# Optimization experiments

Hardware: AMD Instinct MI355X
Metric: run time of the kernel (lower is better)

## Reference

```python
import jax, jax.numpy as jnp
import numpy as np

M, K, N, GROUP = 64, 4096, 11008, 128
NGROUPS = K // GROUP  # 32


def setup_inputs() -> dict:
    key = jax.random.key(0)
    k1, k2, k3, k4, k5 = jax.random.split(key, 5)
    x = jax.random.normal(k1, (M, K), dtype=jnp.float32)
    # packed int4 weights: 8 nibbles per int32, full 32-bit entropy
    qweight = jax.random.bits(k2, (K // 8, N), dtype=jnp.uint32).astype(jnp.int32)
    qzeros = jax.random.bits(k3, (NGROUPS, N // 8), dtype=jnp.uint32).astype(jnp.int32)
    scales = jax.random.uniform(k4, (NGROUPS, N), dtype=jnp.float32, minval=0.001, maxval=0.02)
    bias = jax.random.normal(k5, (N,), dtype=jnp.float32) * 0.01
    return {"x": x, "qweight": qweight, "qzeros": qzeros, "scales": scales, "bias": bias}


def dequantize(qweight, qzeros, scales):
    shifts = jnp.arange(8, dtype=jnp.int32) * 4  # nibble bit offsets 0..28
    # unpack weights: [K//8, N] -> [K//8, 8, N] -> [NGROUPS, GROUP, N]
    w = (jnp.right_shift(qweight[:, None, :], shifts[None, :, None]) & 15)
    w = w.reshape(-1, GROUP, qweight.shape[1])
    # unpack zeros: [NGROUPS, N//8] -> [NGROUPS, N//8, 8] -> [NGROUPS, 1, N]; GPTQ stores zero-1
    z = (jnp.right_shift(qzeros[:, :, None], shifts[None, None, :]) & 15) + 1
    z = z.reshape(z.shape[0], 1, -1)
    # scale * (q - zero), per group: [NGROUPS, GROUP, N] -> [K, N]
    W = scales[:, None, :] * (w - z).astype(scales.dtype)
    return W.reshape(-1, W.shape[2])


def reference(x, qweight, qzeros, scales, bias):
    W = dequantize(qweight, qzeros, scales)  # [K, N] fp32
    return jnp.matmul(x, W.astype(x.dtype)) + bias
```

## Files before the change

### kernel.cpp

```cpp
#include <hip/hip_runtime.h>
#include <hip/hip_bf16.h>

namespace {

constexpr int MM = 64;
constexpr int KK = 4096;
constexpr int NN = 11008;
constexpr int NZROW = NN / 8;
constexpr int BCOL = 128;
constexpr int KSPLIT = 8;
constexpr int KSEG = KK / KSPLIT;
constexpr int BK = 32;
constexpr int NCH = KSEG / BK;
constexpr int NG = KSEG / 128;
constexpr int NT = NN / BCOL;
constexpr int NCHT = KK / BK;
constexpr size_t XBT_OFF = (size_t)KSPLIT * MM * NN * 4;
constexpr size_t WS_NEED = XBT_OFF + (size_t)MM * KK * 2;

typedef float f32x4 __attribute__((ext_vector_type(4)));
typedef short s16x8 __attribute__((ext_vector_type(8)));
typedef int   i32x4 __attribute__((ext_vector_type(4)));

__device__ __forceinline__ int pack_bf16(float a, float b) {
  union { __hip_bfloat162 h; int i; } u;
  u.h.x = __float2bfloat16(a);
  u.h.y = __float2bfloat16(b);
  return u.i;
}

__global__ __launch_bounds__(256) void xcvt_kernel(
    const float* __restrict__ x, unsigned short* __restrict__ xbt)
{
  const int tg = blockIdx.x * 256 + threadIdx.x;
  const int l  = tg & 63;
  const int r  = (tg >> 6) & 3;
  const int ci = tg >> 8;
  const int m  = r * 16 + (l & 15);
  const int k  = ci * BK + (l >> 4) * 8;
  const float* xp = x + (size_t)m * KK + k;
  const f32x4 a0 = *(const f32x4*)xp;
  const f32x4 a1 = *(const f32x4*)(xp + 4);
  i32x4 p;
  p.x = pack_bf16(a0.x, a0.y);
  p.y = pack_bf16(a0.z, a0.w);
  p.z = pack_bf16(a1.x, a1.y);
  p.w = pack_bf16(a1.z, a1.w);
  *(i32x4*)(xbt + (size_t)tg * 8) = p;
}

__global__ __launch_bounds__(256) void prep_kernel(
    const float* __restrict__ bias, float* __restrict__ out)
{
  const int i = blockIdx.x * 256 + threadIdx.x;
  out[i] = bias[i % NN];
}

__global__ __launch_bounds__(256) void reduce_kernel(
    const float* __restrict__ ws, const float* __restrict__ bias,
    float* __restrict__ out)
{
  const int i4 = (blockIdx.x * 256 + threadIdx.x) * 4;
  f32x4 acc = *(const f32x4*)(bias + (i4 % NN));
  #pragma unroll
  for (int s = 0; s < KSPLIT; ++s)
    acc += *(const f32x4*)(ws + (size_t)s * (MM * NN) + i4);
  *(f32x4*)(out + i4) = acc;
}

template<bool WSP>
__global__ __launch_bounds__(256, 4) void gptq_gemm_kernel(
    const float* __restrict__ x, const int* __restrict__ qw,
    const int* __restrict__ qz, const float* __restrict__ scales,
    const unsigned short* __restrict__ xbt, float* __restrict__ out)
{
  const int tid  = threadIdx.x;
  const int wave = tid >> 6;
  const int lane = tid & 63;
  const int c    = lane & 15;
  const int quad = lane >> 4;

  const int ks     = blockIdx.x & 7;
  const int nt     = blockIdx.x >> 3;
  const int n0     = nt * BCOL;
  const int kbase0 = ks * KSEG;
  const int grp0   = kbase0 >> 7;

  const int ncol = n0 + wave * 32 + c;

  const int* qwb = qw + ((size_t)(kbase0 >> 3) + quad) * NN + ncol;
  const unsigned short* xbb = xbt + (size_t)(ks * NCH) * 2048 + lane * 8;
  const float* xab = x + (size_t)c * KK + kbase0 + quad * 8;

  f32x4 acc[8];
  #pragma unroll
  for (int t = 0; t < 8; ++t) acc[t] = {0.f, 0.f, 0.f, 0.f};

  s16x8 pA[2][4];
  int   pB0[4], pB1[4];
  float pS0[2], pS1[2];
  int   pZ0[2], pZ1[2];
  float s0, s1, C0, C1;

  auto ldA = [&](int i) {
    const unsigned short* xp = xbb + (size_t)i * 2048;
    #pragma unroll
    for (int r = 0; r < 4; ++r)
      pA[i & 1][r] = *(const s16x8*)(xp + r * 512);
  };
  auto pfB = [&](int i) {
    const int* qp = qwb + (size_t)i * 4 * NN;
    pB0[i & 3] = qp[0];
    pB1[i & 3] = qp[16];
  };
  auto pfS = [&](int g) {
    const int sl = g & 1;
    const float* sp = scales + (size_t)(grp0 + g) * NN + ncol;
    pS0[sl] = sp[0];
    pS1[sl] = sp[16];
    const int* zp = qz + (size_t)(grp0 + g) * NZROW + (ncol >> 3);
    pZ0[sl] = zp[0];
    pZ1[sl] = zp[2];
  };
  auto setSC = [&](int g) {
    const int sl = g & 1;
    const int sh = (ncol & 7) * 4;
    s0 = pS0[sl];
    s1 = pS1[sl];
    C0 = __int_as_float(0x4B000000 + ((pZ0[sl] >> sh) & 15) + 1);
    C1 = __int_as_float(0x4B000000 + ((pZ1[sl] >> sh) & 15) + 1);
  };
  auto dq8 = [&](int v, float s, float C) -> i32x4 {
    i32x4 p;
    p.x = pack_bf16(s * (__int_as_float(((v      ) & 15) | 0x4B000000) - C),
                    s * (__int_as_float(((v >>  4) & 15) | 0x4B000000) - C));
    p.y = pack_bf16(s * (__int_as_float(((v >>  8) & 15) | 0x4B000000) - C),
                    s * (__int_as_float(((v >> 12) & 15) | 0x4B000000) - C));
    p.z = pack_bf16(s * (__int_as_float(((v >> 16) & 15) | 0x4B000000) - C),
                    s * (__int_as_float(((v >> 20) & 15) | 0x4B000000) - C));
    p.w = pack_bf16(s * (__int_as_float(((v >> 24) & 15) | 0x4B000000) - C),
                    s * (__int_as_float(((v >> 28) & 15) | 0x4B000000) - C));
    return p;
  };
  auto ldA_f32 = [&](int i, int r) -> s16x8 {
    const float* xa = xab + (size_t)r * 16 * KK + i * BK;
    const f32x4 a0 = *(const f32x4*)xa;
    const f32x4 a1 = *(const f32x4*)(xa + 4);
    union { i32x4 i4; s16x8 s8; } ua;
    ua.i4.x = pack_bf16(a0.x, a0.y);
    ua.i4.y = pack_bf16(a0.z, a0.w);
    ua.i4.z = pack_bf16(a1.x, a1.y);
    ua.i4.w = pack_bf16(a1.z, a1.w);
    return ua.s8;
  };

  pfS(0);
  pfB(0); pfB(1); pfB(2);
  if (WSP) ldA(0);
  setSC(0);
  pfS(1);

  #pragma unroll
  for (int i = 0; i < NCH; ++i) {
    if (WSP && i + 1 < NCH) ldA(i + 1);
    if (i + 3 < NCH) pfB(i + 3);

    union { i32x4 i4; s16x8 s8; } u0, u1;
    u0.i4 = dq8(pB0[i & 3], s0, C0);
    u1.i4 = dq8(pB1[i & 3], s1, C1);

    #pragma unroll
    for (int r = 0; r < 4; ++r) {
      const s16x8 af = WSP ? pA[i & 1][r] : ldA_f32(i, r);
      acc[r * 2 + 0] = __builtin_amdgcn_mfma_f32_16x16x32_bf16(af, u0.s8, acc[r * 2 + 0], 0, 0, 0);
      acc[r * 2 + 1] = __builtin_amdgcn_mfma_f32_16x16x32_bf16(af, u1.s8, acc[r * 2 + 1], 0, 0, 0);
    }

    if ((i & 3) == 3) {
      const int g = i >> 2;
      if (g + 1 < NG) { setSC(g + 1); if (g + 2 < NG) pfS(g + 2); }
    }
  }

  if (WSP) {
    float* wsp = out + (size_t)ks * (MM * NN);
    #pragma unroll
    for (int r = 0; r < 4; ++r) {
      #pragma unroll
      for (int t = 0; t < 2; ++t) {
        const f32x4 a = acc[r * 2 + t];
        float* op = wsp + (size_t)(r * 16 + quad * 4) * NN + ncol + t * 16;
        op[0]      = a.x;
        op[NN]     = a.y;
        op[2 * NN] = a.z;
        op[3 * NN] = a.w;
      }
    }
  } else {
    #pragma unroll
    for (int r = 0; r < 4; ++r) {
      #pragma unroll
      for (int t = 0; t < 2; ++t) {
        const f32x4 a = acc[r * 2 + t];
        float* op = out + (size_t)(r * 16 + quad * 4) * NN + ncol + t * 16;
        atomicAdd(&op[0],      a.x);
        atomicAdd(&op[NN],     a.y);
        atomicAdd(&op[2 * NN], a.z);
        atomicAdd(&op[3 * NN], a.w);
      }
    }
  }
}

}

extern "C" void kernel_launch(void* const* d_in, const int* in_sizes, int n_in,
                              void* d_out, int out_size, void* d_ws, size_t ws_size,
                              hipStream_t stream) {
  const float* x      = (const float*)d_in[0];
  const int*   qw     = (const int*)d_in[1];
  const int*   qz     = (const int*)d_in[2];
  const float* scales = (const float*)d_in[3];
  const float* bias   = (const float*)d_in[4];
  float* out = (float*)d_out;

  if (ws_size >= WS_NEED) {
    float* ws = (float*)d_ws;
    unsigned short* xbt = (unsigned short*)((char*)d_ws + XBT_OFF);
    xcvt_kernel<<<(MM * KK / 8) / 256, 256, 0, stream>>>(x, xbt);
    gptq_gemm_kernel<true><<<NT * KSPLIT, 256, 0, stream>>>(x, qw, qz, scales, xbt, ws);
    reduce_kernel<<<(MM * NN) / 1024, 256, 0, stream>>>(ws, bias, out);
  } else {
    prep_kernel<<<(MM * NN) / 256, 256, 0, stream>>>(bias, out);
    gptq_gemm_kernel<false><<<NT * KSPLIT, 256, 0, stream>>>(x, qw, qz, scales, nullptr, out);
  }
}
```

Measured before the change: 102.5 us.

## Fuse x bf16 conversion into GEMM via swizzled LDS staging

Drops the separate xcvt kernel that converted x to a bf16 tiled workspace. Each GEMM block now loads its 64x512 fp32 slice of x, converts it to bf16, and stores it in a 64KB XOR-swizzled shared-memory tile before the main loop. MFMA A-fragments are then read from LDS instead of global memory. This removes one kernel launch and the workspace round trip. In exchange, 64KB of LDS per block likely limits occupancy to about two blocks per CU, and the prologue adds a barrier and redundant x conversion across the 86 N-tiles.

```diff
diff --git a/kernel.cpp b/kernel.cpp
--- a/kernel.cpp
+++ b/kernel.cpp
@@ -14,9 +14,7 @@
 constexpr int NCH = KSEG / BK;
 constexpr int NG = KSEG / 128;
 constexpr int NT = NN / BCOL;
-constexpr int NCHT = KK / BK;
-constexpr size_t XBT_OFF = (size_t)KSPLIT * MM * NN * 4;
-constexpr size_t WS_NEED = XBT_OFF + (size_t)MM * KK * 2;
+constexpr size_t WS_NEED = (size_t)KSPLIT * MM * NN * 4;
 
 typedef float f32x4 __attribute__((ext_vector_type(4)));
 typedef short s16x8 __attribute__((ext_vector_type(8)));
@@ -27,26 +25,6 @@
   u.h.x = __float2bfloat16(a);
   u.h.y = __float2bfloat16(b);
   return u.i;
-}
-
-__global__ __launch_bounds__(256) void xcvt_kernel(
-    const float* __restrict__ x, unsigned short* __restrict__ xbt)
-{
-  const int tg = blockIdx.x * 256 + threadIdx.x;
-  const int l  = tg & 63;
-  const int r  = (tg >> 6) & 3;
-  const int ci = tg >> 8;
-  const int m  = r * 16 + (l & 15);
-  const int k  = ci * BK + (l >> 4) * 8;
-  const float* xp = x + (size_t)m * KK + k;
-  const f32x4 a0 = *(const f32x4*)xp;
-  const f32x4 a1 = *(const f32x4*)(xp + 4);
-  i32x4 p;
-  p.x = pack_bf16(a0.x, a0.y);
-  p.y = pack_bf16(a0.z, a0.w);
-  p.z = pack_bf16(a1.x, a1.y);
-  p.w = pack_bf16(a1.z, a1.w);
-  *(i32x4*)(xbt + (size_t)tg * 8) = p;
 }
 
 __global__ __launch_bounds__(256) void prep_kernel(
@@ -68,12 +46,14 @@
   *(f32x4*)(out + i4) = acc;
 }
 
-template<bool WSP>
+template<bool ATOMIC>
 __global__ __launch_bounds__(256, 4) void gptq_gemm_kernel(
     const float* __restrict__ x, const int* __restrict__ qw,
     const int* __restrict__ qz, const float* __restrict__ scales,
-    const unsigned short* __restrict__ xbt, float* __restrict__ out)
+    float* __restrict__ out)
 {
+  __shared__ int As[16384];
+
   const int tid  = threadIdx.x;
   const int wave = tid >> 6;
   const int lane = tid & 63;
@@ -89,25 +69,16 @@
   const int ncol = n0 + wave * 32 + c;
 
   const int* qwb = qw + ((size_t)(kbase0 >> 3) + quad) * NN + ncol;
-  const unsigned short* xbb = xbt + (size_t)(ks * NCH) * 2048 + lane * 8;
-  const float* xab = x + (size_t)c * KK + kbase0 + quad * 8;
 
   f32x4 acc[8];
   #pragma unroll
   for (int t = 0; t < 8; ++t) acc[t] = {0.f, 0.f, 0.f, 0.f};
 
-  s16x8 pA[2][4];
   int   pB0[4], pB1[4];
   float pS0[2], pS1[2];
   int   pZ0[2], pZ1[2];
   float s0, s1, C0, C1;
 
-  auto ldA = [&](int i) {
-    const unsigned short* xp = xbb + (size_t)i * 2048;
-    #pragma unroll
-    for (int r = 0; r < 4; ++r)
-      pA[i & 1][r] = *(const s16x8*)(xp + r * 512);
-  };
   auto pfB = [&](int i) {
     const int* qp = qwb + (size_t)i * 4 * NN;
     pB0[i & 3] = qp[0];
@@ -142,36 +113,44 @@
                     s * (__int_as_float(((v >> 28) & 15) | 0x4B000000) - C));
     return p;
   };
-  auto ldA_f32 = [&](int i, int r) -> s16x8 {
-    const float* xa = xab + (size_t)r * 16 * KK + i * BK;
-    const f32x4 a0 = *(const f32x4*)xa;
-    const f32x4 a1 = *(const f32x4*)(xa + 4);
-    union { i32x4 i4; s16x8 s8; } ua;
-    ua.i4.x = pack_bf16(a0.x, a0.y);
-    ua.i4.y = pack_bf16(a0.z, a0.w);
-    ua.i4.z = pack_bf16(a1.x, a1.y);
-    ua.i4.w = pack_bf16(a1.z, a1.w);
-    return ua.s8;
-  };
 
   pfS(0);
   pfB(0); pfB(1); pfB(2);
-  if (WSP) ldA(0);
+  pfS(1);
+
+  {
+    const int ciW = lane >> 2;
+    const int cw  = ciW & 7;
+    const int wconst = (ciW * 4 + wave) * 256 + (lane & 3) * 64;
+    const float* xsb = x + (size_t)(wave * 16) * KK + kbase0 + lane * 8;
+    #pragma unroll
+    for (int rr = 0; rr < 16; ++rr) {
+      const float* xp = xsb + (size_t)rr * KK;
+      const f32x4 a0 = *(const f32x4*)xp;
+      const f32x4 a1 = *(const f32x4*)(xp + 4);
+      i32x4 pa;
+      pa.x = pack_bf16(a0.x, a0.y);
+      pa.y = pack_bf16(a0.z, a0.w);
+      pa.z = pack_bf16(a1.x, a1.y);
+      pa.w = pack_bf16(a1.z, a1.w);
+      *(i32x4*)&As[wconst + ((rr ^ cw) << 2)] = pa;
+    }
+  }
+  __asm__ volatile("s_waitcnt lgkmcnt(0)\n\ts_barrier" ::: "memory");
   setSC(0);
-  pfS(1);
 
   #pragma unroll
   for (int i = 0; i < NCH; ++i) {
-    if (WSP && i + 1 < NCH) ldA(i + 1);
     if (i + 3 < NCH) pfB(i + 3);
 
     union { i32x4 i4; s16x8 s8; } u0, u1;
     u0.i4 = dq8(pB0[i & 3], s0, C0);
     u1.i4 = dq8(pB1[i & 3], s1, C1);
 
+    const int rbase = (lane ^ (i & 7)) << 2;
     #pragma unroll
     for (int r = 0; r < 4; ++r) {
-      const s16x8 af = WSP ? pA[i & 1][r] : ldA_f32(i, r);
+      const s16x8 af = *(const s16x8*)&As[rbase + (i * 4 + r) * 256];
       acc[r * 2 + 0] = __builtin_amdgcn_mfma_f32_16x16x32_bf16(af, u0.s8, acc[r * 2 + 0], 0, 0, 0);
       acc[r * 2 + 1] = __builtin_amdgcn_mfma_f32_16x16x32_bf16(af, u1.s8, acc[r * 2 + 1], 0, 0, 0);
     }
@@ -182,7 +161,20 @@
     }
   }
 
-  if (WSP) {
+  if (ATOMIC) {
+    #pragma unroll
+    for (int r = 0; r < 4; ++r) {
+      #pragma unroll
+      for (int t = 0; t < 2; ++t) {
+        const f32x4 a = acc[r * 2 + t];
+        float* op = out + (size_t)(r * 16 + quad * 4) * NN + ncol + t * 16;
+        atomicAdd(&op[0],      a.x);
+        atomicAdd(&op[NN],     a.y);
+        atomicAdd(&op[2 * NN], a.z);
+        atomicAdd(&op[3 * NN], a.w);
+      }
+    }
+  } else {
     float* wsp = out + (size_t)ks * (MM * NN);
     #pragma unroll
     for (int r = 0; r < 4; ++r) {
@@ -196,19 +188,6 @@
         op[3 * NN] = a.w;
       }
     }
-  } else {
-    #pragma unroll
-    for (int r = 0; r < 4; ++r) {
-      #pragma unroll
-      for (int t = 0; t < 2; ++t) {
-        const f32x4 a = acc[r * 2 + t];
-        float* op = out + (size_t)(r * 16 + quad * 4) * NN + ncol + t * 16;
-        atomicAdd(&op[0],      a.x);
-        atomicAdd(&op[NN],     a.y);
-        atomicAdd(&op[2 * NN], a.z);
-        atomicAdd(&op[3 * NN], a.w);
-      }
-    }
   }
 }
 
@@ -226,12 +205,10 @@
 
   if (ws_size >= WS_NEED) {
     float* ws = (float*)d_ws;
-    unsigned short* xbt = (unsigned short*)((char*)d_ws + XBT_OFF);
-    xcvt_kernel<<<(MM * KK / 8) / 256, 256, 0, stream>>>(x, xbt);
-    gptq_gemm_kernel<true><<<NT * KSPLIT, 256, 0, stream>>>(x, qw, qz, scales, xbt, ws);
+    gptq_gemm_kernel<false><<<NT * KSPLIT, 256, 0, stream>>>(x, qw, qz, scales, ws);
     reduce_kernel<<<(MM * NN) / 1024, 256, 0, stream>>>(ws, bias, out);
   } else {
     prep_kernel<<<(MM * NN) / 256, 256, 0, stream>>>(bias, out);
-    gptq_gemm_kernel<false><<<NT * KSPLIT, 256, 0, stream>>>(x, qw, qz, scales, nullptr, out);
-  }
-}
+    gptq_gemm_kernel<true><<<NT * KSPLIT, 256, 0, stream>>>(x, qw, qz, scales, out);
+  }
+}
```

After: 99.91 us. -2.5%, faster.
